# Performance work log

Hardware: AMD Instinct MI355X
Metric: run time of the kernel (lower is better)

Reference implementation:

```python
import jax, jax.numpy as jnp
import numpy as np

B, L, D, H, NL, F, C = 32, 512, 512, 8, 6, 2048, 9
HD = D // H
SCALE = float(np.sqrt(HD))
EPS = 1e-5


def _layernorm(x, g, b):
    mu = jnp.mean(x, axis=-1, keepdims=True)
    var = jnp.mean((x - mu) ** 2, axis=-1, keepdims=True)
    return (x - mu) * jax.lax.rsqrt(var + EPS) * g + b


def setup_inputs() -> dict:
    key = jax.random.key(0)
    ks = jax.random.split(key, 16)
    s = 0.02
    return {
        "x": jax.random.normal(ks[0], (B, L, D), jnp.float32),
        "case_ids": jax.random.randint(ks[1], (B, L), 0, C),
        "attention_mask": jnp.ones((B, L), jnp.int32),
        "Wq": jax.random.normal(ks[2], (NL, D, D), jnp.float32) * s,
        "bq": jnp.zeros((NL, D), jnp.float32),
        "Wk": jax.random.normal(ks[3], (NL, D, D), jnp.float32) * s,
        "bk": jnp.zeros((NL, D), jnp.float32),
        "Wv": jax.random.normal(ks[4], (NL, D, D), jnp.float32) * s,
        "bv": jnp.zeros((NL, D), jnp.float32),
        "Wo": jax.random.normal(ks[5], (NL, D, D), jnp.float32) * s,
        "bo": jnp.zeros((NL, D), jnp.float32),
        "ln1_g": jnp.ones((NL, D), jnp.float32),
        "ln1_b": jnp.zeros((NL, D), jnp.float32),
        "ln2_g": jnp.ones((NL, D), jnp.float32),
        "ln2_b": jnp.zeros((NL, D), jnp.float32),
        "W1": jax.random.normal(ks[6], (NL, D, F), jnp.float32) * s,
        "b1": jnp.zeros((NL, F), jnp.float32),
        "W2": jax.random.normal(ks[7], (NL, F, D), jnp.float32) * s,
        "b2": jnp.zeros((NL, D), jnp.float32),
        "case_bias": jax.random.normal(ks[8], (NL, H, C, C), jnp.float32) * 0.1,
        "verb_bias": jax.random.normal(ks[9], (NL, H), jnp.float32) * 0.1,
        "fn_g": jnp.ones((D,), jnp.float32),
        "fn_b": jnp.zeros((D,), jnp.float32),
    }


def reference(x, case_ids, attention_mask, Wq, bq, Wk, bk, Wv, bv, Wo, bo,
              ln1_g, ln1_b, ln2_g, ln2_b, W1, b1, W2, b2,
              case_bias, verb_bias, fn_g, fn_b):
    dt = x.dtype
    # causal + padding additive mask: [B, 1, L, L]
    causal = jnp.triu(jnp.full((L, L), -10000.0, dtype=dt), k=1)[None, None]
    pad = (1.0 - attention_mask.astype(dt))[:, None, None, :] * -10000.0
    mask = causal + pad
    verb_mask = (case_ids == 8).astype(dt)  # [B, L]
    ci, cj = case_ids[:, :, None], case_ids[:, None, :]  # [B,L,1], [B,1,L]

    for i in range(NL):
        h = _layernorm(x, ln1_g[i], ln1_b[i])
        q = (h @ Wq[i] + bq[i]).reshape(B, L, H, HD).transpose(0, 2, 1, 3)
        k = (h @ Wk[i] + bk[i]).reshape(B, L, H, HD).transpose(0, 2, 1, 3)
        v = (h @ Wv[i] + bv[i]).reshape(B, L, H, HD).transpose(0, 2, 1, 3)
        scores = jnp.einsum('bhqd,bhkd->bhqk', q, k) / SCALE
        # Panini grammatical bias: per-head pairwise case bias + verb key bias
        pbias = case_bias[i][:, ci, cj]  # [H, B, L, L]
        scores = scores + jnp.transpose(pbias, (1, 0, 2, 3))
        scores = scores + verb_bias[i][None, :, None, None] * verb_mask[:, None, None, :]
        scores = scores + mask
        w = jax.nn.softmax(scores, axis=-1)
        attn = jnp.einsum('bhqk,bhkd->bhqd', w, v).transpose(0, 2, 1, 3).reshape(B, L, D)
        x = x + attn @ Wo[i] + bo[i]
        h2 = _layernorm(x, ln2_g[i], ln2_b[i])
        ff = jax.nn.gelu(h2 @ W1[i] + b1[i], approximate=False) @ W2[i] + b2[i]
        x = x + ff
    return _layernorm(x, fn_g, fn_b)
```

## Files before the change

kernel.cpp:

```cpp
#include <hip/hip_runtime.h>
#include <hip/hip_bf16.h>

#define B_   32
#define L_   512
#define D_   512
#define H_   8
#define NL_  6
#define F_   2048
#define C_   9
#define HD_  64
#define MTOK 16384

typedef __bf16 bf16x8 __attribute__((ext_vector_type(8)));
typedef __bf16 bf16x4 __attribute__((ext_vector_type(4)));
typedef float  f32x4  __attribute__((ext_vector_type(4)));

#define MFMA16(a,b,c) __builtin_amdgcn_mfma_f32_16x16x32_bf16((a),(b),(c),0,0,0)
#define GLD16(g,l) __builtin_amdgcn_global_load_lds( \
    (const __attribute__((address_space(1))) void*)(g), \
    (__attribute__((address_space(3))) void*)(l), 16, 0, 0)

__global__ __launch_bounds__(256) void transpose_w(
    const float* __restrict__ in, __hip_bfloat16* __restrict__ out,
    int K, int N, size_t zso)
{
    __shared__ float t[32][33];
    const int z = blockIdx.z;
    const float* src = in + (size_t)z * K * N;
    __hip_bfloat16* dst = out + (size_t)z * zso;
    const int n0 = blockIdx.x * 32, k0 = blockIdx.y * 32;
    const int tx = threadIdx.x, ty = threadIdx.y;
#pragma unroll
    for (int r = ty; r < 32; r += 8)
        t[r][tx] = src[(size_t)(k0 + r) * N + n0 + tx];
    __syncthreads();
#pragma unroll
    for (int r = ty; r < 32; r += 8)
        dst[(size_t)(n0 + r) * K + k0 + tx] = __float2bfloat16(t[tx][r]);
}

__global__ void cvt_f32_bf16(const float4* __restrict__ in,
                             __hip_bfloat16* __restrict__ out, int n8)
{
    int i = blockIdx.x * blockDim.x + threadIdx.x;
    if (i >= n8) return;
    float4 a = in[2 * i], b = in[2 * i + 1];
    bf16x8 o;
    o[0] = (__bf16)a.x; o[1] = (__bf16)a.y; o[2] = (__bf16)a.z; o[3] = (__bf16)a.w;
    o[4] = (__bf16)b.x; o[5] = (__bf16)b.y; o[6] = (__bf16)b.z; o[7] = (__bf16)b.w;
    *(bf16x8*)(out + (size_t)i * 8) = o;
}

__global__ __launch_bounds__(256) void bias_build(
    const int* __restrict__ case_ids, const int* __restrict__ amask,
    const float* __restrict__ cbias, const float* __restrict__ vbias,
    __hip_bfloat16* __restrict__ tab)
{
    const unsigned idx = blockIdx.x * 256 + threadIdx.x;
    const int kv = idx & 511;
    unsigned r = idx >> 9;
    const int ci = r % 9; r /= 9;
    const int hh = r % H_; r /= H_;
    const int b = r % B_; const int l = r / B_;
    const int cj = case_ids[b * L_ + kv];
    const float v = cbias[(((size_t)l * H_ + hh) * C_ + ci) * C_ + cj]
                  + (cj == 8 ? vbias[l * H_ + hh] : 0.f)
                  - 10000.f * (1.f - (float)amask[b * L_ + kv]);
    tab[idx] = __float2bfloat16(v);
}

template <typename OUT>
__global__ __launch_bounds__(256) void ln_kernel(
    const __hip_bfloat16* __restrict__ x, const float* __restrict__ g,
    const float* __restrict__ be, OUT* __restrict__ out)
{
    const int row  = blockIdx.x * 4 + (threadIdx.x >> 6);
    const int lane = threadIdx.x & 63;
    const int c0   = lane * 8;
    const bf16x8 xv = *(const bf16x8*)(x + (size_t)row * D_ + c0);
    float v[8];
#pragma unroll
    for (int j = 0; j < 8; ++j) v[j] = (float)xv[j];

    float s = 0.f;
#pragma unroll
    for (int j = 0; j < 8; ++j) s += v[j];
#pragma unroll
    for (int o = 1; o < 64; o <<= 1) s += __shfl_xor(s, o, 64);
    const float mu = s * (1.0f / D_);

    float s2 = 0.f;
#pragma unroll
    for (int j = 0; j < 8; ++j) { float d = v[j] - mu; s2 += d * d; }
#pragma unroll
    for (int o = 1; o < 64; o <<= 1) s2 += __shfl_xor(s2, o, 64);
    const float rs = rsqrtf(s2 * (1.0f / D_) + 1e-5f);

    float4 g0 = *(const float4*)(g + c0);
    float4 g1 = *(const float4*)(g + c0 + 4);
    float4 b0 = *(const float4*)(be + c0);
    float4 b1 = *(const float4*)(be + c0 + 4);
    float gg[8] = {g0.x, g0.y, g0.z, g0.w, g1.x, g1.y, g1.z, g1.w};
    float bb[8] = {b0.x, b0.y, b0.z, b0.w, b1.x, b1.y, b1.z, b1.w};

    if constexpr (sizeof(OUT) == 2) {
        bf16x8 o8;
#pragma unroll
        for (int j = 0; j < 8; ++j)
            o8[j] = (__bf16)((v[j] - mu) * rs * gg[j] + bb[j]);
        *(bf16x8*)((__hip_bfloat16*)out + (size_t)row * D_ + c0) = o8;
    } else {
        float* op = (float*)out + (size_t)row * D_ + c0;
        float4 r0, r1;
        r0.x = (v[0]-mu)*rs*gg[0]+bb[0]; r0.y = (v[1]-mu)*rs*gg[1]+bb[1];
        r0.z = (v[2]-mu)*rs*gg[2]+bb[2]; r0.w = (v[3]-mu)*rs*gg[3]+bb[3];
        r1.x = (v[4]-mu)*rs*gg[4]+bb[4]; r1.y = (v[5]-mu)*rs*gg[5]+bb[5];
        r1.z = (v[6]-mu)*rs*gg[6]+bb[6]; r1.w = (v[7]-mu)*rs*gg[7]+bb[7];
        *(float4*)op = r0; *(float4*)(op + 4) = r1;
    }
}

__device__ __forceinline__ float gelu_tanh(float v)
{
    const float t2 = v * v;
    const float u  = v * (0.7978845608028654f + 0.0356774081363001f * t2);
    const float a  = __builtin_fabsf(u);
    const float e  = __expf(-2.0f * a);
    const float r  = __builtin_amdgcn_rcpf(1.0f + e);
    const float th = (1.0f - e) * r;
    return 0.5f * v + 0.5f * __builtin_fabsf(v) * th;
}

template <int EPI, int WM>
__global__ __launch_bounds__(WM * 128, (WM == 4) ? 4 : 3) void gemm_r5(
    const __hip_bfloat16* __restrict__ A,
    const __hip_bfloat16* __restrict__ BT,
    const float* __restrict__ bias0, const float* __restrict__ bias1,
    const float* __restrict__ bias2,
    void* __restrict__ out0, void* __restrict__ out1, void* __restrict__ out2,
    const __hip_bfloat16* __restrict__ Res, int Ndim, int K)
{
    constexpr int THREADS = WM * 128;
    constexpr int BM = WM * 64;
    __shared__ __align__(16) __hip_bfloat16 As[3][BM * 32];
    __shared__ __align__(16) __hip_bfloat16 Bs[3][128 * 32];

    const int tid = threadIdx.x;
    const int w = tid >> 6, lane = tid & 63;
    const int lq = lane & 15, lg = lane >> 4;
    const int wm = w >> 1, wn = w & 1;
    const int RB = wm * 64, CB = wn * 64;

    const int gX = gridDim.x;
    const int nwg = gX * gridDim.y;
    int flat = blockIdx.y * gX + blockIdx.x;
    {
        const int qq = nwg >> 3, rr = nwg & 7;
        const int xcd = flat & 7, off = flat >> 3;
        flat = (xcd < rr ? xcd * (qq + 1) : rr * (qq + 1) + (xcd - rr) * qq) + off;
    }
    const int bx = flat % gX, by = flat / gX;
    const int m0 = by * BM, n0 = bx * 128;

    const int rc = tid >> 2;
    const int sc = ((tid & 3) ^ ((rc >> 1) & 3)) * 8;
    const __hip_bfloat16* gA0 = A  + (size_t)(m0 + rc) * K + sc;
    const __hip_bfloat16* gB0 = BT + (size_t)(n0 + rc) * K + sc;

    auto STAGE = [&](int tt) {
        const size_t ko = (size_t)tt * 32;
        const int sl = tt % 3;
        char* ab = (char*)As[sl] + w * 1024;
        GLD16(gA0 + ko, ab);
        GLD16(gA0 + (size_t)(THREADS / 4) * K + ko, ab + THREADS * 16);
        char* bb = (char*)Bs[sl] + w * 1024;
        GLD16(gB0 + ko, bb);
        if constexpr (WM == 2)
            GLD16(gB0 + (size_t)64 * K + ko, bb + 4096);
    };

    const int rsw = (lq >> 1) & 3;
    const int aoff = (RB + lq) * 64 + ((lg ^ rsw) << 4);
    const int boff = (CB + lq) * 64 + ((lg ^ rsw) << 4);

    f32x4 acc[4][4] = {};
    const int NTt = K >> 5;

    STAGE(0); STAGE(1);

    for (int t = 0; t < NTt; ++t) {
        if (t + 1 < NTt) {
            if constexpr (WM == 4) asm volatile("s_waitcnt vmcnt(3)" ::: "memory");
            else                   asm volatile("s_waitcnt vmcnt(4)" ::: "memory");
        } else {
            asm volatile("s_waitcnt vmcnt(0)" ::: "memory");
        }
        __builtin_amdgcn_s_barrier();
        __builtin_amdgcn_sched_barrier(0);

        const char* ca = (const char*)As[t % 3];
        const char* cb = (const char*)Bs[t % 3];
        bf16x8 af[4], bf[4];
#pragma unroll
        for (int fm = 0; fm < 4; ++fm) af[fm] = *(const bf16x8*)(ca + aoff + fm * 1024);
#pragma unroll
        for (int fn = 0; fn < 4; ++fn) bf[fn] = *(const bf16x8*)(cb + boff + fn * 1024);

        if (t + 2 < NTt) STAGE(t + 2);

        __builtin_amdgcn_s_setprio(1);
#pragma unroll
        for (int fm = 0; fm < 4; ++fm)
#pragma unroll
            for (int fn = 0; fn < 4; ++fn)
                acc[fm][fn] = MFMA16(af[fm], bf[fn], acc[fm][fn]);
        __builtin_amdgcn_s_setprio(0);
    }

    if constexpr (EPI == 4) {
        const int sec = n0 >> 9;
        const int nb = (n0 & 511) + CB;
        const float* bp = sec == 0 ? bias0 : (sec == 1 ? bias1 : bias2);
        float bcol[4];
#pragma unroll
        for (int fn = 0; fn < 4; ++fn) bcol[fn] = bp[nb + fn * 16 + lq];
        if (sec < 2) {
            __hip_bfloat16* op = (__hip_bfloat16*)(sec == 0 ? out0 : out1);
#pragma unroll
            for (int fm = 0; fm < 4; ++fm)
#pragma unroll
                for (int fn = 0; fn < 4; ++fn)
#pragma unroll
                    for (int r = 0; r < 4; ++r) {
                        const int m = m0 + RB + fm * 16 + lg * 4 + r;
                        op[(size_t)m * 512 + nb + fn * 16 + lq] =
                            __float2bfloat16(acc[fm][fn][r] + bcol[fn]);
                    }
        } else {
            __hip_bfloat16* vp = (__hip_bfloat16*)out2;
            const int bb = m0 >> 9;
            const int l0 = (m0 & 511) + RB + lg * 4;
#pragma unroll
            for (int fm = 0; fm < 4; ++fm)
#pragma unroll
                for (int fn = 0; fn < 4; ++fn) {
                    bf16x4 pv;
#pragma unroll
                    for (int r = 0; r < 4; ++r)
                        pv[r] = (__bf16)(acc[fm][fn][r] + bcol[fn]);
                    *(bf16x4*)(vp + ((size_t)(bb * 512 + nb + fn * 16 + lq)) * 512
                               + l0 + fm * 16) = pv;
                }
        }
    } else {
        float bcol[4];
#pragma unroll
        for (int fn = 0; fn < 4; ++fn) bcol[fn] = bias0[n0 + CB + fn * 16 + lq];
#pragma unroll
        for (int fm = 0; fm < 4; ++fm)
#pragma unroll
            for (int fn = 0; fn < 4; ++fn) {
                const int n = n0 + CB + fn * 16 + lq;
#pragma unroll
                for (int r = 0; r < 4; ++r) {
                    const int m = m0 + RB + fm * 16 + lg * 4 + r;
                    float v = acc[fm][fn][r] + bcol[fn];
                    if constexpr (EPI == 1) {
                        __hip_bfloat16* Co = (__hip_bfloat16*)out0;
                        const size_t idx = (size_t)m * Ndim + n;
                        Co[idx] = __float2bfloat16((float)Res[idx] + v);
                    } else {
                        ((__hip_bfloat16*)out0)[(size_t)m * Ndim + n] =
                            __float2bfloat16(gelu_tanh(v));
                    }
                }
            }
    }
}

__global__ __launch_bounds__(256, 4) void attn_kernel(
    const __hip_bfloat16* __restrict__ Q, const __hip_bfloat16* __restrict__ K,
    const __hip_bfloat16* __restrict__ VT, __hip_bfloat16* __restrict__ Out,
    const int* __restrict__ case_ids, const __hip_bfloat16* __restrict__ tab,
    int layer)
{
    __shared__ __align__(16) __bf16 Ks[2][64 * 64];
    __shared__ __align__(16) __bf16 Vs[2][64 * 64];
    __shared__ __align__(16) __bf16 Pl[4][16 * 64];

    const int bh = blockIdx.x;
    const int b = bh >> 3, hh = bh & 7;
    const int qcA = blockIdx.y;
    const int qcB = 7 - qcA;
    const int t = threadIdx.x;
    const int w = t >> 6, lane = t & 63;
    const int lq = lane & 15, lg = lane >> 4;
    const int swz = lq & 7;

    const int rA = w * 16 + (lane >> 3);
    const int swsrc = ((lane & 7) ^ (lane >> 3)) << 4;
    const __hip_bfloat16* kg0 = K  + ((size_t)b * L_ + rA) * D_ + hh * HD_;
    const __hip_bfloat16* vg0 = VT + ((size_t)b * D_ + hh * HD_ + rA) * L_;

    auto stage = [&](int buf, int kv0) {
        const char* gk = (const char*)(kg0 + (size_t)kv0 * D_) + swsrc;
        GLD16(gk,                      (char*)Ks[buf] + w * 2048);
        GLD16(gk + (size_t)8 * D_ * 2, (char*)Ks[buf] + w * 2048 + 1024);
        const char* gv = (const char*)(vg0 + kv0) + swsrc;
        GLD16(gv,                      (char*)Vs[buf] + w * 2048);
        GLD16(gv + (size_t)8 * L_ * 2, (char*)Vs[buf] + w * 2048 + 1024);
    };

    stage(0, 0);

    const int qloc = w * 16 + lq;
    const int qrowA = qcA * 64 + qloc;
    const int qrowB = qcB * 64 + qloc;
    const size_t tbase = (((size_t)layer * B_ + b) * H_ + hh) * C_;
    const __hip_bfloat16* ciqA = tab + (tbase + case_ids[b * L_ + qrowA]) * L_;
    const __hip_bfloat16* ciqB = tab + (tbase + case_ids[b * L_ + qrowB]) * L_;

    const __hip_bfloat16* qpA = Q + ((size_t)b * L_ + qrowA) * D_ + hh * HD_;
    const __hip_bfloat16* qpB = Q + ((size_t)b * L_ + qrowB) * D_ + hh * HD_;
    const bf16x8 qfA0 = *(const bf16x8*)(qpA + lg * 8);
    const bf16x8 qfA1 = *(const bf16x8*)(qpA + 32 + lg * 8);
    const bf16x8 qfB0 = *(const bf16x8*)(qpB + lg * 8);
    const bf16x8 qfB1 = *(const bf16x8*)(qpB + 32 + lg * 8);

    float mA = -1e30f, lA = 0.f, mB = -1e30f, lB = 0.f;
    f32x4 oA[4] = {}, oB[4] = {};
    int cur = 0;

    auto process = [&](const bf16x8 qf0, const bf16x8 qf1,
                       const __hip_bfloat16* ciq, int qcX,
                       float& m_run, float& l_run, f32x4* o,
                       const char* kb, const char* vb2, int kt) {
        bf16x4 bb[4];
#pragma unroll
        for (int c = 0; c < 4; ++c)
            bb[c] = *(const bf16x4*)(ciq + kt * 64 + 16 * c + lg * 4);

        f32x4 s[4] = {};
        __builtin_amdgcn_s_setprio(1);
#pragma unroll
        for (int c = 0; c < 4; ++c) {
            const bf16x8 ka = *(const bf16x8*)(kb + (16 * c + lq) * 128 + ((lg ^ swz) << 4));
            s[c] = MFMA16(ka, qf0, s[c]);
            const bf16x8 kc = *(const bf16x8*)(kb + (16 * c + lq) * 128 + (((4 + lg) ^ swz) << 4));
            s[c] = MFMA16(kc, qf1, s[c]);
        }
        __builtin_amdgcn_s_setprio(0);

        const bool dtile = (kt == qcX);
        float xs[16];
#pragma unroll
        for (int c = 0; c < 4; ++c)
#pragma unroll
            for (int r = 0; r < 4; ++r) {
                const int kvl = 16 * c + lg * 4 + r;
                float v = s[c][r] * 0.125f + (float)bb[c][r];
                xs[4 * c + r] = (dtile && (kvl > qloc)) ? -1e9f : v;
            }

        float a0 = fmaxf(fmaxf(xs[0], xs[1]),  fmaxf(xs[2], xs[3]));
        float a1 = fmaxf(fmaxf(xs[4], xs[5]),  fmaxf(xs[6], xs[7]));
        float a2 = fmaxf(fmaxf(xs[8], xs[9]),  fmaxf(xs[10], xs[11]));
        float a3 = fmaxf(fmaxf(xs[12], xs[13]), fmaxf(xs[14], xs[15]));
        float pmax = fmaxf(fmaxf(a0, a1), fmaxf(a2, a3));
        pmax = fmaxf(pmax, __shfl_xor(pmax, 16, 64));
        pmax = fmaxf(pmax, __shfl_xor(pmax, 32, 64));

        const float mnew = fmaxf(m_run, pmax);
        const float corr = __expf(m_run - mnew);
        float ps = 0.f;
#pragma unroll
        for (int j = 0; j < 16; ++j) { xs[j] = __expf(xs[j] - mnew); ps += xs[j]; }
        ps += __shfl_xor(ps, 16, 64);
        ps += __shfl_xor(ps, 32, 64);
        l_run = l_run * corr + ps;
        m_run = mnew;

        float cr[4];
#pragma unroll
        for (int r = 0; r < 4; ++r) cr[r] = __shfl(corr, lg * 4 + r, 64);
#pragma unroll
        for (int nt = 0; nt < 4; ++nt)
#pragma unroll
            for (int r = 0; r < 4; ++r) o[nt][r] *= cr[r];

        char* pw = (char*)Pl[w];
#pragma unroll
        for (int c = 0; c < 4; ++c) {
            bf16x4 pv;
#pragma unroll
            for (int r = 0; r < 4; ++r) pv[r] = (__bf16)xs[4 * c + r];
            const int slot = (2 * c + (lg >> 1)) ^ swz;
            *(bf16x4*)(pw + lq * 128 + (slot << 4) + ((lg & 1) << 3)) = pv;
        }

        __builtin_amdgcn_s_setprio(1);
#pragma unroll
        for (int hf = 0; hf < 2; ++hf) {
            const bf16x8 pf = *(const bf16x8*)(pw + lq * 128 + (((hf * 4 + lg) ^ swz) << 4));
#pragma unroll
            for (int nt = 0; nt < 4; ++nt) {
                const bf16x8 vf = *(const bf16x8*)(vb2 + (nt * 16 + lq) * 128
                                                   + (((hf * 4 + lg) ^ swz) << 4));
                o[nt] = MFMA16(pf, vf, o[nt]);
            }
        }
        __builtin_amdgcn_s_setprio(0);
    };

    for (int kt = 0; kt <= qcB; ++kt) {
        if (kt) __builtin_amdgcn_s_barrier();
        if (kt < qcB) {
            stage(cur ^ 1, (kt + 1) * 64);
            asm volatile("s_waitcnt vmcnt(4)" ::: "memory");
        } else {
            asm volatile("s_waitcnt vmcnt(0)" ::: "memory");
        }
        __builtin_amdgcn_s_barrier();
        __builtin_amdgcn_sched_barrier(0);

        const char* kb  = (const char*)Ks[cur];
        const char* vb2 = (const char*)Vs[cur];

        process(qfB0, qfB1, ciqB, qcB, mB, lB, oB, kb, vb2, kt);
        if (kt <= qcA)
            process(qfA0, qfA1, ciqA, qcA, mA, lA, oA, kb, vb2, kt);
        cur ^= 1;
    }

    auto writeout = [&](float l_run, f32x4* o, int qcX) {
        const float inv = 1.f / l_run;
        float ir[4];
#pragma unroll
        for (int r = 0; r < 4; ++r) ir[r] = __shfl(inv, lg * 4 + r, 64);
        __hip_bfloat16* op = Out + ((size_t)b * L_ + qcX * 64 + w * 16) * D_ + hh * HD_;
#pragma unroll
        for (int nt = 0; nt < 4; ++nt)
#pragma unroll
            for (int r = 0; r < 4; ++r)
                op[(size_t)(lg * 4 + r) * D_ + nt * 16 + lq] =
                    __float2bfloat16(o[nt][r] * ir[r]);
    };
    writeout(lA, oA, qcA);
    writeout(lB, oB, qcB);
}

extern "C" void kernel_launch(void* const* d_in, const int* in_sizes, int n_in,
                              void* d_out, int out_size, void* d_ws, size_t ws_size,
                              hipStream_t stream)
{
    const float* x_in  = (const float*)d_in[0];
    const int*   cids  = (const int*)  d_in[1];
    const int*   amask = (const int*)  d_in[2];
    const float* Wq = (const float*)d_in[3];
    const float* bq = (const float*)d_in[4];
    const float* Wk = (const float*)d_in[5];
    const float* bk = (const float*)d_in[6];
    const float* Wv = (const float*)d_in[7];
    const float* bv = (const float*)d_in[8];
    const float* Wo = (const float*)d_in[9];
    const float* bo = (const float*)d_in[10];
    const float* ln1g = (const float*)d_in[11];
    const float* ln1b = (const float*)d_in[12];
    const float* ln2g = (const float*)d_in[13];
    const float* ln2b = (const float*)d_in[14];
    const float* W1 = (const float*)d_in[15];
    const float* b1 = (const float*)d_in[16];
    const float* W2 = (const float*)d_in[17];
    const float* b2 = (const float*)d_in[18];
    const float* cbias = (const float*)d_in[19];
    const float* vbias = (const float*)d_in[20];
    const float* fng = (const float*)d_in[21];
    const float* fnb = (const float*)d_in[22];

    char* w = (char*)d_ws;
    __hip_bfloat16* x_ws = (__hip_bfloat16*)w;  w += (size_t)MTOK * D_ * 2;
    __hip_bfloat16* hbuf = (__hip_bfloat16*)w;  w += (size_t)MTOK * D_ * 2;
    __hip_bfloat16* qbuf = (__hip_bfloat16*)w;  w += (size_t)MTOK * D_ * 2;
    __hip_bfloat16* kbuf = (__hip_bfloat16*)w;  w += (size_t)MTOK * D_ * 2;
    __hip_bfloat16* vtb  = (__hip_bfloat16*)w;  w += (size_t)MTOK * D_ * 2;
    __hip_bfloat16* ffb  = (__hip_bfloat16*)w;  w += (size_t)MTOK * F_ * 2;
    __hip_bfloat16* WqkvT = (__hip_bfloat16*)w; w += (size_t)NL_ * 3 * D_ * D_ * 2;
    __hip_bfloat16* WoT  = (__hip_bfloat16*)w;  w += (size_t)NL_ * D_ * D_ * 2;
    __hip_bfloat16* W1T  = (__hip_bfloat16*)w;  w += (size_t)NL_ * D_ * F_ * 2;
    __hip_bfloat16* W2T  = (__hip_bfloat16*)w;  w += (size_t)NL_ * D_ * F_ * 2;
    __hip_bfloat16* btab = (__hip_bfloat16*)w;  w += (size_t)NL_ * B_ * H_ * C_ * L_ * 2;

    const size_t qkvZ = (size_t)3 * D_ * D_;
    const dim3 tb(32, 8);
    transpose_w<<<dim3(D_/32, D_/32, NL_), tb, 0, stream>>>(Wq, WqkvT,           D_, D_, qkvZ);
    transpose_w<<<dim3(D_/32, D_/32, NL_), tb, 0, stream>>>(Wk, WqkvT + D_*D_,   D_, D_, qkvZ);
    transpose_w<<<dim3(D_/32, D_/32, NL_), tb, 0, stream>>>(Wv, WqkvT + 2*D_*D_, D_, D_, qkvZ);
    transpose_w<<<dim3(D_/32, D_/32, NL_), tb, 0, stream>>>(Wo, WoT, D_, D_, (size_t)D_*D_);
    transpose_w<<<dim3(F_/32, D_/32, NL_), tb, 0, stream>>>(W1, W1T, D_, F_, (size_t)D_*F_);
    transpose_w<<<dim3(D_/32, F_/32, NL_), tb, 0, stream>>>(W2, W2T, F_, D_, (size_t)D_*F_);

    bias_build<<<(NL_ * B_ * H_ * C_ * L_) / 256, 256, 0, stream>>>(
        cids, amask, cbias, vbias, btab);

    cvt_f32_bf16<<<4096, 256, 0, stream>>>((const float4*)x_in, x_ws,
                                           MTOK * D_ / 8);

    const dim3 gQKV(12, 128);
    const dim3 gO(4, 128);
    const dim3 gW1(16, 64);
    const dim3 gW2(4, 128);

    for (int i = 0; i < NL_; ++i) {
        ln_kernel<__hip_bfloat16><<<MTOK/4, 256, 0, stream>>>(
            x_ws, ln1g + i * D_, ln1b + i * D_, hbuf);

        gemm_r5<4, 2><<<gQKV, 256, 0, stream>>>(hbuf, WqkvT + (size_t)i * qkvZ,
            bq + i*D_, bk + i*D_, bv + i*D_, qbuf, kbuf, vtb, nullptr, 512, D_);

        attn_kernel<<<dim3(B_ * H_, 4), 256, 0, stream>>>(
            qbuf, kbuf, vtb, hbuf, cids, btab, i);

        gemm_r5<1, 2><<<gO, 256, 0, stream>>>(hbuf, WoT + (size_t)i*D_*D_,
            bo + i*D_, nullptr, nullptr, x_ws, nullptr, nullptr, x_ws, D_, D_);

        ln_kernel<__hip_bfloat16><<<MTOK/4, 256, 0, stream>>>(
            x_ws, ln2g + i * D_, ln2b + i * D_, hbuf);

        gemm_r5<2, 4><<<gW1, 512, 0, stream>>>(hbuf, W1T + (size_t)i*D_*F_,
            b1 + i*F_, nullptr, nullptr, ffb, nullptr, nullptr, nullptr, F_, D_);

        gemm_r5<1, 2><<<gW2, 256, 0, stream>>>(ffb, W2T + (size_t)i*D_*F_,
            b2 + i*D_, nullptr, nullptr, x_ws, nullptr, nullptr, x_ws, D_, F_);
    }

    ln_kernel<float><<<MTOK/4, 256, 0, stream>>>(x_ws, fng, fnb, (float*)d_out);
}
```

Baseline: 1.219 ms.

## Add 256x128-tile GEMM with 4 waves for Wo, W1 and W2 projections

```diff
diff --git a/kernel.cpp b/kernel.cpp
--- a/kernel.cpp
+++ b/kernel.cpp
@@ -132,7 +132,7 @@
 }
 
 template <int EPI, int WM>
-__global__ __launch_bounds__(WM * 128, (WM == 4) ? 4 : 3) void gemm_r5(
+__global__ __launch_bounds__(WM * 128, 3) void gemm_r5(
     const __hip_bfloat16* __restrict__ A,
     const __hip_bfloat16* __restrict__ BT,
     const float* __restrict__ bias0, const float* __restrict__ bias1,
@@ -175,8 +175,7 @@
         GLD16(gA0 + (size_t)(THREADS / 4) * K + ko, ab + THREADS * 16);
         char* bb = (char*)Bs[sl] + w * 1024;
         GLD16(gB0 + ko, bb);
-        if constexpr (WM == 2)
-            GLD16(gB0 + (size_t)64 * K + ko, bb + 4096);
+        GLD16(gB0 + (size_t)64 * K + ko, bb + 4096);
     };
 
     const int rsw = (lq >> 1) & 3;
@@ -190,8 +189,7 @@
 
     for (int t = 0; t < NTt; ++t) {
         if (t + 1 < NTt) {
-            if constexpr (WM == 4) asm volatile("s_waitcnt vmcnt(3)" ::: "memory");
-            else                   asm volatile("s_waitcnt vmcnt(4)" ::: "memory");
+            asm volatile("s_waitcnt vmcnt(4)" ::: "memory");
         } else {
             asm volatile("s_waitcnt vmcnt(0)" ::: "memory");
         }
@@ -217,65 +215,147 @@
         __builtin_amdgcn_s_setprio(0);
     }
 
-    if constexpr (EPI == 4) {
-        const int sec = n0 >> 9;
-        const int nb = (n0 & 511) + CB;
-        const float* bp = sec == 0 ? bias0 : (sec == 1 ? bias1 : bias2);
-        float bcol[4];
-#pragma unroll
-        for (int fn = 0; fn < 4; ++fn) bcol[fn] = bp[nb + fn * 16 + lq];
-        if (sec < 2) {
-            __hip_bfloat16* op = (__hip_bfloat16*)(sec == 0 ? out0 : out1);
-#pragma unroll
-            for (int fm = 0; fm < 4; ++fm)
-#pragma unroll
-                for (int fn = 0; fn < 4; ++fn)
-#pragma unroll
-                    for (int r = 0; r < 4; ++r) {
-                        const int m = m0 + RB + fm * 16 + lg * 4 + r;
-                        op[(size_t)m * 512 + nb + fn * 16 + lq] =
-                            __float2bfloat16(acc[fm][fn][r] + bcol[fn]);
-                    }
-        } else {
-            __hip_bfloat16* vp = (__hip_bfloat16*)out2;
-            const int bb = m0 >> 9;
-            const int l0 = (m0 & 511) + RB + lg * 4;
-#pragma unroll
-            for (int fm = 0; fm < 4; ++fm)
-#pragma unroll
-                for (int fn = 0; fn < 4; ++fn) {
-                    bf16x4 pv;
-#pragma unroll
-                    for (int r = 0; r < 4; ++r)
-                        pv[r] = (__bf16)(acc[fm][fn][r] + bcol[fn]);
-                    *(bf16x4*)(vp + ((size_t)(bb * 512 + nb + fn * 16 + lq)) * 512
-                               + l0 + fm * 16) = pv;
-                }
-        }
-    } else {
-        float bcol[4];
-#pragma unroll
-        for (int fn = 0; fn < 4; ++fn) bcol[fn] = bias0[n0 + CB + fn * 16 + lq];
+    const int sec = n0 >> 9;
+    const int nb = (n0 & 511) + CB;
+    const float* bp = sec == 0 ? bias0 : (sec == 1 ? bias1 : bias2);
+    float bcol[4];
+#pragma unroll
+    for (int fn = 0; fn < 4; ++fn) bcol[fn] = bp[nb + fn * 16 + lq];
+    if (sec < 2) {
+        __hip_bfloat16* op = (__hip_bfloat16*)(sec == 0 ? out0 : out1);
 #pragma unroll
         for (int fm = 0; fm < 4; ++fm)
 #pragma unroll
-            for (int fn = 0; fn < 4; ++fn) {
-                const int n = n0 + CB + fn * 16 + lq;
+            for (int fn = 0; fn < 4; ++fn)
 #pragma unroll
                 for (int r = 0; r < 4; ++r) {
                     const int m = m0 + RB + fm * 16 + lg * 4 + r;
-                    float v = acc[fm][fn][r] + bcol[fn];
-                    if constexpr (EPI == 1) {
-                        __hip_bfloat16* Co = (__hip_bfloat16*)out0;
-                        const size_t idx = (size_t)m * Ndim + n;
-                        Co[idx] = __float2bfloat16((float)Res[idx] + v);
-                    } else {
-                        ((__hip_bfloat16*)out0)[(size_t)m * Ndim + n] =
-                            __float2bfloat16(gelu_tanh(v));
-                    }
+                    op[(size_t)m * 512 + nb + fn * 16 + lq] =
+                        __float2bfloat16(acc[fm][fn][r] + bcol[fn]);
+                }
+    } else {
+        __hip_bfloat16* vp = (__hip_bfloat16*)out2;
+        const int bb = m0 >> 9;
+        const int l0 = (m0 & 511) + RB + lg * 4;
+#pragma unroll
+        for (int fm = 0; fm < 4; ++fm)
+#pragma unroll
+            for (int fn = 0; fn < 4; ++fn) {
+                bf16x4 pv;
+#pragma unroll
+                for (int r = 0; r < 4; ++r)
+                    pv[r] = (__bf16)(acc[fm][fn][r] + bcol[fn]);
+                *(bf16x4*)(vp + ((size_t)(bb * 512 + nb + fn * 16 + lq)) * 512
+                           + l0 + fm * 16) = pv;
+            }
+    }
+}
+
+template <int EPI>
+__global__ __launch_bounds__(256, 2) void gemm_v2(
+    const __hip_bfloat16* __restrict__ A,
+    const __hip_bfloat16* __restrict__ BT,
+    const float* __restrict__ bias0,
+    void* __restrict__ out0,
+    const __hip_bfloat16* __restrict__ Res, int Ndim, int K)
+{
+    __shared__ __align__(16) __hip_bfloat16 As[3][256 * 32];
+    __shared__ __align__(16) __hip_bfloat16 Bs[3][128 * 32];
+
+    const int tid = threadIdx.x;
+    const int w = tid >> 6, lane = tid & 63;
+    const int lq = lane & 15, lg = lane >> 4;
+    const int wm = w >> 1, wn = w & 1;
+    const int RB = wm * 128, CB = wn * 64;
+
+    const int gX = gridDim.x;
+    const int nwg = gX * gridDim.y;
+    int flat = blockIdx.y * gX + blockIdx.x;
+    {
+        const int qq = nwg >> 3, rr = nwg & 7;
+        const int xcd = flat & 7, off = flat >> 3;
+        flat = (xcd < rr ? xcd * (qq + 1) : rr * (qq + 1) + (xcd - rr) * qq) + off;
+    }
+    const int bx = flat % gX, by = flat / gX;
+    const int m0 = by * 256, n0 = bx * 128;
+
+    const int rr_ = w * 16 + (lane >> 2);
+    const int sc = ((lane & 3) ^ ((lane >> 3) & 3)) * 8;
+    const __hip_bfloat16* gA0 = A  + (size_t)(m0 + rr_) * K + sc;
+    const __hip_bfloat16* gB0 = BT + (size_t)(n0 + rr_) * K + sc;
+
+    auto STAGE = [&](int tt) {
+        const size_t ko = (size_t)tt * 32;
+        const int sl = tt % 3;
+        char* ab = (char*)As[sl] + w * 1024;
+        GLD16(gA0 + ko,                   ab);
+        GLD16(gA0 + (size_t)64 * K + ko,  ab + 4096);
+        GLD16(gA0 + (size_t)128 * K + ko, ab + 8192);
+        GLD16(gA0 + (size_t)192 * K + ko, ab + 12288);
+        char* bb = (char*)Bs[sl] + w * 1024;
+        GLD16(gB0 + ko,                   bb);
+        GLD16(gB0 + (size_t)64 * K + ko,  bb + 4096);
+    };
+
+    const int rsw = (lq >> 1) & 3;
+    const int aoff = (RB + lq) * 64 + ((lg ^ rsw) << 4);
+    const int boff = (CB + lq) * 64 + ((lg ^ rsw) << 4);
+
+    f32x4 acc[8][4] = {};
+    const int NTt = K >> 5;
+
+    STAGE(0); STAGE(1);
+
+    for (int t = 0; t < NTt; ++t) {
+        if (t + 1 < NTt) {
+            asm volatile("s_waitcnt vmcnt(6)" ::: "memory");
+        } else {
+            asm volatile("s_waitcnt vmcnt(0)" ::: "memory");
+        }
+        __builtin_amdgcn_s_barrier();
+        __builtin_amdgcn_sched_barrier(0);
+
+        const char* ca = (const char*)As[t % 3];
+        const char* cb = (const char*)Bs[t % 3];
+        bf16x8 af[8], bf[4];
+#pragma unroll
+        for (int fm = 0; fm < 8; ++fm) af[fm] = *(const bf16x8*)(ca + aoff + fm * 1024);
+#pragma unroll
+        for (int fn = 0; fn < 4; ++fn) bf[fn] = *(const bf16x8*)(cb + boff + fn * 1024);
+
+        if (t + 2 < NTt) STAGE(t + 2);
+
+        __builtin_amdgcn_s_setprio(1);
+#pragma unroll
+        for (int fm = 0; fm < 8; ++fm)
+#pragma unroll
+            for (int fn = 0; fn < 4; ++fn)
+                acc[fm][fn] = MFMA16(af[fm], bf[fn], acc[fm][fn]);
+        __builtin_amdgcn_s_setprio(0);
+    }
+
+    float bcol[4];
+#pragma unroll
+    for (int fn = 0; fn < 4; ++fn) bcol[fn] = bias0[n0 + CB + fn * 16 + lq];
+#pragma unroll
+    for (int fm = 0; fm < 8; ++fm)
+#pragma unroll
+        for (int fn = 0; fn < 4; ++fn) {
+            const int n = n0 + CB + fn * 16 + lq;
+#pragma unroll
+            for (int r = 0; r < 4; ++r) {
+                const int m = m0 + RB + fm * 16 + lg * 4 + r;
+                float v = acc[fm][fn][r] + bcol[fn];
+                if constexpr (EPI == 1) {
+                    __hip_bfloat16* Co = (__hip_bfloat16*)out0;
+                    const size_t idx = (size_t)m * Ndim + n;
+                    Co[idx] = __float2bfloat16((float)Res[idx] + v);
+                } else {
+                    ((__hip_bfloat16*)out0)[(size_t)m * Ndim + n] =
+                        __float2bfloat16(gelu_tanh(v));
                 }
             }
-    }
+        }
 }
 
 __global__ __launch_bounds__(256, 4) void attn_kernel(
@@ -506,9 +586,9 @@
                                            MTOK * D_ / 8);
 
     const dim3 gQKV(12, 128);
-    const dim3 gO(4, 128);
+    const dim3 gO(4, 64);
     const dim3 gW1(16, 64);
-    const dim3 gW2(4, 128);
+    const dim3 gW2(4, 64);
 
     for (int i = 0; i < NL_; ++i) {
         ln_kernel<__hip_bfloat16><<<MTOK/4, 256, 0, stream>>>(
@@ -520,17 +600,17 @@
         attn_kernel<<<dim3(B_ * H_, 4), 256, 0, stream>>>(
             qbuf, kbuf, vtb, hbuf, cids, btab, i);
 
-        gemm_r5<1, 2><<<gO, 256, 0, stream>>>(hbuf, WoT + (size_t)i*D_*D_,
-            bo + i*D_, nullptr, nullptr, x_ws, nullptr, nullptr, x_ws, D_, D_);
+        gemm_v2<1><<<gO, 256, 0, stream>>>(hbuf, WoT + (size_t)i*D_*D_,
+            bo + i*D_, x_ws, x_ws, D_, D_);
 
         ln_kernel<__hip_bfloat16><<<MTOK/4, 256, 0, stream>>>(
             x_ws, ln2g + i * D_, ln2b + i * D_, hbuf);
 
-        gemm_r5<2, 4><<<gW1, 512, 0, stream>>>(hbuf, W1T + (size_t)i*D_*F_,
-            b1 + i*F_, nullptr, nullptr, ffb, nullptr, nullptr, nullptr, F_, D_);
-
-        gemm_r5<1, 2><<<gW2, 256, 0, stream>>>(ffb, W2T + (size_t)i*D_*F_,
-            b2 + i*D_, nullptr, nullptr, x_ws, nullptr, nullptr, x_ws, D_, F_);
+        gemm_v2<2><<<gW1, 256, 0, stream>>>(hbuf, W1T + (size_t)i*D_*F_,
+            b1 + i*F_, ffb, nullptr, F_, D_);
+
+        gemm_v2<1><<<gW2, 256, 0, stream>>>(ffb, W2T + (size_t)i*D_*F_,
+            b2 + i*D_, x_ws, x_ws, D_, F_);
     }
 
     ln_kernel<float><<<MTOK/4, 256, 0, stream>>>(x_ws, fng, fnb, (float*)d_out);
```

Result: slower. 1.275 ms (+4.6%).
